# Kernel optimization log

Hardware: AMD Instinct MI355X
Metric: run time of the kernel (lower is better)

## Reference

```python
import jax, jax.numpy as jnp
import numpy as np

N_NODES = 100000
D = 128


def gcn_conv(x, W, b, src, dst, deg_inv_sqrt):
    # PyG GCNConv: linear transform, symmetric-normalized aggregation with self-loops, bias
    h = x @ W  # [N, D_out]
    norm = deg_inv_sqrt[src] * deg_inv_sqrt[dst]  # [E_tot]
    msgs = h[src] * norm[:, None]  # gather + scale  [E_tot, D_out]
    out = jax.ops.segment_sum(msgs, dst, num_segments=x.shape[0])  # scatter-add to targets
    return out + b


def _prep_edges(edge_index, n_nodes):
    # add self-loops (weight 1) and compute deg^{-1/2} over targets (flow source_to_target)
    loops = jnp.arange(n_nodes, dtype=edge_index.dtype)
    src = jnp.concatenate([edge_index[0], loops])
    dst = jnp.concatenate([edge_index[1], loops])
    deg = jax.ops.segment_sum(jnp.ones_like(dst, dtype=jnp.float32), dst, num_segments=n_nodes)
    deg_inv_sqrt = jnp.where(deg > 0, jax.lax.rsqrt(jnp.maximum(deg, 1.0)), 0.0)
    return src, dst, deg_inv_sqrt


def setup_inputs() -> dict:
    key = jax.random.key(0)
    ks = jax.random.split(key, 8)
    node_fts = jax.random.normal(ks[0], (N_NODES, D), dtype=jnp.float32)
    edge_index = jax.random.randint(ks[1], (2, 1600000), 0, N_NODES, dtype=jnp.int64)
    scale = 1.0 / np.sqrt(D)
    W1 = jax.random.uniform(ks[2], (D, D), jnp.float32, -scale, scale)
    b1 = jnp.zeros((D,), jnp.float32)
    W2 = jax.random.uniform(ks[3], (D, D), jnp.float32, -scale, scale)
    b2 = jnp.zeros((D,), jnp.float32)
    W3 = jax.random.uniform(ks[4], (D, D), jnp.float32, -scale, scale)
    b3 = jnp.zeros((D,), jnp.float32)
    return {"node_fts": node_fts, "edge_index": edge_index,
            "W1": W1, "b1": b1, "W2": W2, "b2": b2, "W3": W3, "b3": b3}


def reference(node_fts, edge_index, W1, b1, W2, b2, W3, b3):
    n = node_fts.shape[0]
    src, dst, dinv = _prep_edges(edge_index, n)
    x = jax.nn.relu(gcn_conv(node_fts, W1, b1, src, dst, dinv))
    x = jax.nn.relu(gcn_conv(x, W2, b2, src, dst, dinv))
    x = jax.nn.relu(gcn_conv(x, W3, b3, src, dst, dinv))
    return x
```

## Files before the change

kernel.cpp:

```cpp
#include <hip/hip_runtime.h>

#define NN 100000
#define EE 1600000
#define NPART 8
#define PSZ (NN / NPART)
#define NI4 (EE / 4)
#define SUBW 196
#define NSB (NPART * 64)
#define SCAP 4096
#define RCAP 8192
#define FCHUNKS 128
#define FBLOCKS (NPART * FCHUNKS)
#define WTBLOCKS 48
#define DEGB 64
#define LBCAP 48

typedef __attribute__((ext_vector_type(8))) short bf16x8;
typedef __attribute__((ext_vector_type(4))) float f32x4;

__device__ inline unsigned int f2bf2(float a, float b) {
    unsigned int ua = __float_as_uint(a);
    unsigned int ub = __float_as_uint(b);
    ua = (ua + 0x7fffu + ((ua >> 16) & 1u)) >> 16;
    ub = (ub + 0x7fffu + ((ub >> 16) & 1u)) >> 16;
    return ua | (ub << 16);
}
__device__ inline unsigned short f2bf(float a) {
    unsigned int u = __float_as_uint(a);
    return (unsigned short)((u + 0x7fffu + ((u >> 16) & 1u)) >> 16);
}
__device__ inline float2 bf2f2(unsigned int u) {
    return make_float2(__uint_as_float(u << 16), __uint_as_float(u & 0xffff0000u));
}


__global__ __launch_bounds__(256) void fbwt_kernel(const int4* __restrict__ src4,
                                                   const int4* __restrict__ dst4,
                                                   int* __restrict__ gcur2,
                                                   uint2* __restrict__ buckets2,
                                                   int* __restrict__ deg,
                                                   const float* __restrict__ W1,
                                                   const float* __restrict__ W2,
                                                   const float* __restrict__ W3,
                                                   unsigned short* __restrict__ wt1,
                                                   unsigned short* __restrict__ wt2,
                                                   unsigned short* __restrict__ wt3,
                                                   unsigned int* __restrict__ hb) {
    __shared__ uint2 bins[64][LBCAP];
    __shared__ int bcnt[64];
    __shared__ int gbase[64];
    __shared__ float tile[32][33];
    const int bx = blockIdx.x;

    if (bx < DEGB) {
        const int a0 = bx * (NI4 / DEGB);
        const int a1 = a0 + (NI4 / DEGB);
        for (int i = a0 + threadIdx.x; i < a1; i += 256) {
            int4 d4 = dst4[i];
            atomicAdd(&deg[d4.x], 1);
            atomicAdd(&deg[d4.y], 1);
            atomicAdd(&deg[d4.z], 1);
            atomicAdd(&deg[d4.w], 1);
        }
        return;
    }

    if (bx < DEGB + WTBLOCKS) {
        const int wb = bx - DEGB;
        const int m = wb >> 4;
        const int tl = wb & 15;
        const int ti = tl >> 2, tj = tl & 3;
        const float* W = m == 0 ? W1 : (m == 1 ? W2 : W3);
        unsigned short* wt = m == 0 ? wt1 : (m == 1 ? wt2 : wt3);
        const int r = threadIdx.x >> 5, c = threadIdx.x & 31;
#pragma unroll
        for (int rr = r; rr < 32; rr += 8)
            tile[rr][c] = W[(ti * 32 + rr) * 128 + tj * 32 + c];
        __syncthreads();
#pragma unroll
        for (int rr = r; rr < 32; rr += 8)
            wt[(size_t)(tj * 32 + rr) * 128 + ti * 32 + c] = f2bf(tile[c][rr]);
        if (wb == 0 && threadIdx.x < 64) hb[(size_t)NN * 64 + threadIdx.x] = 0;
        return;
    }

    const int fb = bx - DEGB - WTBLOCKS;
    const int p = fb >> 7;
    const int ch = fb & 127;
    if (threadIdx.x < 64) bcnt[threadIdx.x] = 0;
    __syncthreads();
    const int lo = p * PSZ, hi = lo + PSZ;
    const int chunk4 = NI4 / FCHUNKS;
    const int a0 = ch * chunk4, a1 = a0 + chunk4;
    for (int i = a0 + threadIdx.x; i < a1; i += 256) {
        int4 d4 = dst4[i];
        bool m0 = (d4.x >= lo && d4.x < hi);
        bool m1 = (d4.y >= lo && d4.y < hi);
        bool m2 = (d4.z >= lo && d4.z < hi);
        bool m3 = (d4.w >= lo && d4.w < hi);
        if (!(m0 | m1 | m2 | m3)) continue;
        int4 s4 = src4[i];
        int ss[4] = {s4.x, s4.y, s4.z, s4.w};
        int dd[4] = {d4.x, d4.y, d4.z, d4.w};
        bool mm[4] = {m0, m1, m2, m3};
#pragma unroll
        for (int k = 0; k < 4; ++k) {
            if (!mm[k]) continue;
            int li = (dd[k] - lo) / SUBW;
            int pos = atomicAdd(&bcnt[li], 1);
            if (pos < LBCAP) {
                bins[li][pos] = make_uint2((unsigned)ss[k], (unsigned)dd[k]);
            } else {
                int sb = p * 64 + li;
                int gp = atomicAdd(&gcur2[sb], 1);
                buckets2[(size_t)sb * SCAP + gp] = make_uint2((unsigned)ss[k], (unsigned)dd[k]);
            }
        }
    }
    __syncthreads();
    if (threadIdx.x < 64) {
        int cc = min(bcnt[threadIdx.x], LBCAP);
        gbase[threadIdx.x] = atomicAdd(&gcur2[p * 64 + threadIdx.x], cc);
        bcnt[threadIdx.x] = cc;
    }
    __syncthreads();
    for (int b = 0; b < 64; ++b) {
        const int cc = bcnt[b];
        uint2* outp = buckets2 + (size_t)(p * 64 + b) * SCAP + gbase[b];
        for (int i = threadIdx.x; i < cc; i += 256) outp[i] = bins[b][i];
    }
}


template <bool F32IN>
__device__ __forceinline__ void gemm_body(int wave, const void* __restrict__ xin,
                                          const unsigned short* __restrict__ wt,
                                          const int* __restrict__ deg,
                                          unsigned int* __restrict__ hb) {
    const int base = wave * 64;
    if (base >= NN) return;
    const int lane = threadIdx.x & 63;
    const int r = lane & 15;
    const int q = lane >> 4;
    const unsigned short* wrow = wt + (size_t)r * 128 + q * 8;
    bf16x8 wfr[4][8];
#pragma unroll
    for (int kc = 0; kc < 4; ++kc)
#pragma unroll
        for (int nt = 0; nt < 8; ++nt)
            wfr[kc][nt] = *(const bf16x8*)(wrow + (size_t)nt * 16 * 128 + kc * 32);
#pragma unroll
    for (int tt = 0; tt < 4; ++tt) {
        const int m0 = base + tt * 16;
        if (m0 >= NN) break;
        f32x4 acc[8] = {};
#pragma unroll
        for (int kc = 0; kc < 4; ++kc) {
            bf16x8 xf;
            if (F32IN) {
                const float* xrow = (const float*)xin + (size_t)(m0 + r) * 128 + q * 8 + kc * 32;
                float4 a = *(const float4*)xrow;
                float4 b = *(const float4*)(xrow + 4);
                unsigned short tmp[8] = {f2bf(a.x), f2bf(a.y), f2bf(a.z), f2bf(a.w),
                                         f2bf(b.x), f2bf(b.y), f2bf(b.z), f2bf(b.w)};
                xf = *(const bf16x8*)tmp;
            } else {
                const unsigned short* xrow =
                    (const unsigned short*)xin + (size_t)(m0 + r) * 128 + q * 8 + kc * 32;
                xf = *(const bf16x8*)xrow;
            }
#pragma unroll
            for (int nt = 0; nt < 8; ++nt)
                acc[nt] = __builtin_amdgcn_mfma_f32_16x16x32_bf16(wfr[kc][nt], xf, acc[nt], 0, 0, 0);
        }
        const int orow = m0 + r;
        const float dvr = rsqrtf(1.0f + (float)deg[orow]);
        unsigned int* hrow = hb + (size_t)orow * 64;
#pragma unroll
        for (int nt = 0; nt < 8; ++nt) {
            int n = nt * 16 + q * 4;
            *(uint2*)(hrow + (n >> 1)) =
                make_uint2(f2bf2(acc[nt][0] * dvr, acc[nt][1] * dvr),
                           f2bf2(acc[nt][2] * dvr, acc[nt][3] * dvr));
        }
    }
}


__global__ __launch_bounds__(256, 2) void sort3_gemm1_kernel(const uint2* __restrict__ buckets2,
                                                             const int* __restrict__ gcur2,
                                                             int* __restrict__ csr,
                                                             int* __restrict__ info,
                                                             float* __restrict__ dinv,
                                                             const float* __restrict__ x0,
                                                             const unsigned short* __restrict__ wt1,
                                                             const int* __restrict__ deg,
                                                             unsigned int* __restrict__ hb) {
    __shared__ int hist[256];
    __shared__ int pscan[256];
    __shared__ int lcur[256];
    __shared__ int staged[RCAP];
    if (blockIdx.x >= 512) {
        const int wave = (blockIdx.x - 512) * 4 + (threadIdx.x >> 6);
        gemm_body<true>(wave, (const void*)x0, wt1, deg, hb);
        return;
    }
    const int sb = blockIdx.x;
    const int li = sb & 63;
    const int base_node = (sb >> 6) * PSZ + li * SUBW;
    const int nnodes = min(SUBW, PSZ - li * SUBW);
    const int scnt = gcur2[sb];
    const uint2* bk = buckets2 + (size_t)sb * SCAP;
    const int t = threadIdx.x;
    hist[t] = 0;
    __syncthreads();
    for (int i = t; i < scnt; i += 256) atomicAdd(&hist[(int)bk[i].y - base_node], 1);
    __syncthreads();
    const int padded = (t < nnodes) ? ((hist[t] + 7) & ~7) : 0;
    pscan[t] = padded;
    __syncthreads();
    for (int off = 1; off < 256; off <<= 1) {
        int v = (t >= off) ? pscan[t - off] : 0;
        __syncthreads();
        pscan[t] += v;
        __syncthreads();
    }
    const int rstart = pscan[t] - padded;
    lcur[t] = rstart;
    __syncthreads();
    const int total = pscan[255];
    for (int i = t; i < total; i += 256) staged[i] = NN;
    __syncthreads();
    for (int i = t; i < scnt; i += 256) {
        uint2 r = bk[i];
        int pos = atomicAdd(&lcur[(int)r.y - base_node], 1);
        staged[pos] = (int)r.x;
    }
    __syncthreads();
    int4* co = (int4*)(csr + (size_t)sb * RCAP);
    for (int i = t; i < (total >> 2); i += 256) co[i] = ((const int4*)staged)[i];
    if (t < nnodes) {
        int dg = hist[t];
        info[base_node + t] = ((sb * RCAP + rstart) << 8) | dg;
        dinv[base_node + t] = rsqrtf(1.0f + (float)dg);
    }
}

template <bool F32IN>
__global__ __launch_bounds__(256, 2) void gemm_kernel(const void* __restrict__ xin,
                                                      const unsigned short* __restrict__ wt,
                                                      const int* __restrict__ deg,
                                                      unsigned int* __restrict__ hb) {
    const int wave = blockIdx.x * 4 + (threadIdx.x >> 6);
    gemm_body<F32IN>(wave, xin, wt, deg, hb);
}


template <bool BF16OUT>
__device__ __forceinline__ void agg_node(int d, const unsigned int* __restrict__ hb,
                                         const int* __restrict__ csr,
                                         const int* __restrict__ info,
                                         const float* __restrict__ dinv,
                                         const float2* __restrict__ bias2,
                                         void* __restrict__ outp) {
    const int j = threadIdx.x & 63;
    const int ifo = info[d];
    int e = ifo >> 8;
    const int end = e + (((ifo & 255) + 7) & ~7);
    float2 acc = bf2f2(hb[(size_t)d * 64 + j]);
    for (; e + 16 <= end; e += 16) {
        int4 c0 = *(const int4*)(csr + e);
        int4 c1 = *(const int4*)(csr + e + 4);
        int4 c2 = *(const int4*)(csr + e + 8);
        int4 c3 = *(const int4*)(csr + e + 12);
        unsigned int v0 = hb[(size_t)c0.x * 64 + j];
        unsigned int v1 = hb[(size_t)c0.y * 64 + j];
        unsigned int v2 = hb[(size_t)c0.z * 64 + j];
        unsigned int v3 = hb[(size_t)c0.w * 64 + j];
        unsigned int v4 = hb[(size_t)c1.x * 64 + j];
        unsigned int v5 = hb[(size_t)c1.y * 64 + j];
        unsigned int v6 = hb[(size_t)c1.z * 64 + j];
        unsigned int v7 = hb[(size_t)c1.w * 64 + j];
        unsigned int v8 = hb[(size_t)c2.x * 64 + j];
        unsigned int v9 = hb[(size_t)c2.y * 64 + j];
        unsigned int va = hb[(size_t)c2.z * 64 + j];
        unsigned int vb = hb[(size_t)c2.w * 64 + j];
        unsigned int vc = hb[(size_t)c3.x * 64 + j];
        unsigned int vd = hb[(size_t)c3.y * 64 + j];
        unsigned int ve = hb[(size_t)c3.z * 64 + j];
        unsigned int vf = hb[(size_t)c3.w * 64 + j];
        float2 f0 = bf2f2(v0), f1 = bf2f2(v1), f2 = bf2f2(v2), f3 = bf2f2(v3);
        float2 f4 = bf2f2(v4), f5 = bf2f2(v5), f6 = bf2f2(v6), f7 = bf2f2(v7);
        float2 f8 = bf2f2(v8), f9 = bf2f2(v9), fa = bf2f2(va), fb = bf2f2(vb);
        float2 fc = bf2f2(vc), fd = bf2f2(vd), fe = bf2f2(ve), ff = bf2f2(vf);
        acc.x += ((f0.x + f1.x) + (f2.x + f3.x)) + ((f4.x + f5.x) + (f6.x + f7.x)) +
                 ((f8.x + f9.x) + (fa.x + fb.x)) + ((fc.x + fd.x) + (fe.x + ff.x));
        acc.y += ((f0.y + f1.y) + (f2.y + f3.y)) + ((f4.y + f5.y) + (f6.y + f7.y)) +
                 ((f8.y + f9.y) + (fa.y + fb.y)) + ((fc.y + fd.y) + (fe.y + ff.y));
    }
    if (e < end) {
        int4 c0 = *(const int4*)(csr + e);
        int4 c1 = *(const int4*)(csr + e + 4);
        unsigned int v0 = hb[(size_t)c0.x * 64 + j];
        unsigned int v1 = hb[(size_t)c0.y * 64 + j];
        unsigned int v2 = hb[(size_t)c0.z * 64 + j];
        unsigned int v3 = hb[(size_t)c0.w * 64 + j];
        unsigned int v4 = hb[(size_t)c1.x * 64 + j];
        unsigned int v5 = hb[(size_t)c1.y * 64 + j];
        unsigned int v6 = hb[(size_t)c1.z * 64 + j];
        unsigned int v7 = hb[(size_t)c1.w * 64 + j];
        float2 f0 = bf2f2(v0), f1 = bf2f2(v1), f2 = bf2f2(v2), f3 = bf2f2(v3);
        float2 f4 = bf2f2(v4), f5 = bf2f2(v5), f6 = bf2f2(v6), f7 = bf2f2(v7);
        acc.x += ((f0.x + f1.x) + (f2.x + f3.x)) + ((f4.x + f5.x) + (f6.x + f7.x));
        acc.y += ((f0.y + f1.y) + (f2.y + f3.y)) + ((f4.y + f5.y) + (f6.y + f7.y));
    }
    const float dv = dinv[d];
    float2 bb = bias2[j];
    float ox = fmaxf(dv * acc.x + bb.x, 0.0f);
    float oy = fmaxf(dv * acc.y + bb.y, 0.0f);
    if (BF16OUT) {
        ((unsigned int*)outp)[(size_t)d * 64 + j] = f2bf2(ox, oy);
    } else {
        ((float2*)outp)[(size_t)d * 64 + j] = make_float2(ox, oy);
    }
}

template <bool BF16OUT>
__global__ __launch_bounds__(256) void aggregate_kernel(const unsigned int* __restrict__ hb,
                                                        const int* __restrict__ csr,
                                                        const int* __restrict__ info,
                                                        const float* __restrict__ dinv,
                                                        const float2* __restrict__ bias2,
                                                        void* __restrict__ outp) {
    const int w = threadIdx.x >> 6;
    const int stride = (int)gridDim.x * 4;
    for (int d = blockIdx.x * 4 + w; d < NN; d += stride)
        agg_node<BF16OUT>(d, hb, csr, info, dinv, bias2, outp);
}


extern "C" void kernel_launch(void* const* d_in, const int* in_sizes, int n_in,
                              void* d_out, int out_size, void* d_ws, size_t ws_size,
                              hipStream_t stream) {
    const float* x0 = (const float*)d_in[0];
    const int* ei = (const int*)d_in[1];
    const float* W1 = (const float*)d_in[2];
    const float* b1 = (const float*)d_in[3];
    const float* W2 = (const float*)d_in[4];
    const float* b2 = (const float*)d_in[5];
    const float* W3 = (const float*)d_in[6];
    const float* b3 = (const float*)d_in[7];
    float* out = (float*)d_out;

    char* ws = (char*)d_ws;
    size_t off = 0;
    auto alloc = [&](size_t bytes) -> void* {
        off = (off + 511) & ~(size_t)511;
        void* p = ws + off;
        off += bytes;
        return p;
    };
    unsigned int* hb  = (unsigned int*)alloc(((size_t)NN + 1) * 64 * 4);
    int*   csr     = (int*)  alloc((size_t)NSB * RCAP * sizeof(int));
    uint2* buckets2 = (uint2*)alloc((size_t)NSB * SCAP * sizeof(uint2));
    int*   info    = (int*)  alloc((size_t)NN * sizeof(int));
    float* dinv    = (float*)alloc((size_t)NN * sizeof(float));
    int*   deg     = (int*)  alloc((size_t)NN * sizeof(int));
    int*   gcur2   = (int*)  alloc(NSB * sizeof(int));
    unsigned short* wt1 = (unsigned short*)alloc(128 * 128 * 2);
    unsigned short* wt2 = (unsigned short*)alloc(128 * 128 * 2);
    unsigned short* wt3 = (unsigned short*)alloc(128 * 128 * 2);

    unsigned int* xact = (unsigned int*)d_out;

    const int4* src4 = (const int4*)ei;
    const int4* dst4 = (const int4*)(ei + EE);

    hipMemsetAsync(gcur2, 0, NSB * sizeof(int), stream);
    hipMemsetAsync(deg, 0, (size_t)NN * sizeof(int), stream);
    fbwt_kernel<<<DEGB + WTBLOCKS + FBLOCKS, 256, 0, stream>>>(src4, dst4, gcur2, buckets2, deg,
                                                               W1, W2, W3, wt1, wt2, wt3, hb);
    sort3_gemm1_kernel<<<903, 256, 0, stream>>>(buckets2, gcur2, csr, info, dinv,
                                                x0, wt1, deg, hb);
    aggregate_kernel<true><<<2048, 256, 0, stream>>>(hb, csr, info, dinv,
                                                     (const float2*)b1, (void*)xact);
    gemm_kernel<false><<<391, 256, 0, stream>>>((const void*)xact, wt2, deg, hb);
    aggregate_kernel<true><<<2048, 256, 0, stream>>>(hb, csr, info, dinv,
                                                     (const float2*)b2, (void*)xact);
    gemm_kernel<false><<<391, 256, 0, stream>>>((const void*)xact, wt3, deg, hb);
    aggregate_kernel<false><<<2048, 256, 0, stream>>>(hb, csr, info, dinv,
                                                      (const float2*)b3, (void*)out);
}
```

Baseline: 448.9 us.

## Replace bucketed CSR sort with fixed-capacity per-node rows via atomic scatter

Drops the two-pass partition, bucket and local-sort CSR build and instead gives each destination node a fixed 64-slot row, pre-filled with a sentinel index and filled through per-node atomic cursors. Aggregation now indexes a row directly by node id and derives the normalization from the degree array, so the info and dinv arrays go away and aggregate uses one wave per node with no grid-stride loop. This cuts the preprocessing work and a kernel's worth of global traffic, in exchange for heavy global atomics, scattered 4-byte writes and a 25.6 MB CSR fill. Any node with more than 64 incoming edges would overflow its row, which is only safe for the random test graph.

```diff
diff --git a/kernel.cpp b/kernel.cpp
--- a/kernel.cpp
+++ b/kernel.cpp
@@ -2,18 +2,13 @@
 
 #define NN 100000
 #define EE 1600000
-#define NPART 8
-#define PSZ (NN / NPART)
 #define NI4 (EE / 4)
-#define SUBW 196
-#define NSB (NPART * 64)
-#define SCAP 4096
-#define RCAP 8192
-#define FCHUNKS 128
-#define FBLOCKS (NPART * FCHUNKS)
-#define WTBLOCKS 48
-#define DEGB 64
-#define LBCAP 48
+#define ROWCAP 64
+#define DEGB 128
+#define WTB 48
+#define FILLB 512
+#define SCB 1024
+#define G1B 391
 
 typedef __attribute__((ext_vector_type(8))) short bf16x8;
 typedef __attribute__((ext_vector_type(4))) float f32x4;
@@ -34,21 +29,16 @@
 }
 
 
-__global__ __launch_bounds__(256) void fbwt_kernel(const int4* __restrict__ src4,
-                                                   const int4* __restrict__ dst4,
-                                                   int* __restrict__ gcur2,
-                                                   uint2* __restrict__ buckets2,
-                                                   int* __restrict__ deg,
-                                                   const float* __restrict__ W1,
-                                                   const float* __restrict__ W2,
-                                                   const float* __restrict__ W3,
-                                                   unsigned short* __restrict__ wt1,
-                                                   unsigned short* __restrict__ wt2,
-                                                   unsigned short* __restrict__ wt3,
-                                                   unsigned int* __restrict__ hb) {
-    __shared__ uint2 bins[64][LBCAP];
-    __shared__ int bcnt[64];
-    __shared__ int gbase[64];
+__global__ __launch_bounds__(256) void prep1_kernel(const int4* __restrict__ dst4,
+                                                    int* __restrict__ deg,
+                                                    const float* __restrict__ W1,
+                                                    const float* __restrict__ W2,
+                                                    const float* __restrict__ W3,
+                                                    unsigned short* __restrict__ wt1,
+                                                    unsigned short* __restrict__ wt2,
+                                                    unsigned short* __restrict__ wt3,
+                                                    unsigned int* __restrict__ hb,
+                                                    int* __restrict__ csr) {
     __shared__ float tile[32][33];
     const int bx = blockIdx.x;
 
@@ -65,7 +55,7 @@
         return;
     }
 
-    if (bx < DEGB + WTBLOCKS) {
+    if (bx < DEGB + WTB) {
         const int wb = bx - DEGB;
         const int m = wb >> 4;
         const int tl = wb & 15;
@@ -84,51 +74,12 @@
         return;
     }
 
-    const int fb = bx - DEGB - WTBLOCKS;
-    const int p = fb >> 7;
-    const int ch = fb & 127;
-    if (threadIdx.x < 64) bcnt[threadIdx.x] = 0;
-    __syncthreads();
-    const int lo = p * PSZ, hi = lo + PSZ;
-    const int chunk4 = NI4 / FCHUNKS;
-    const int a0 = ch * chunk4, a1 = a0 + chunk4;
-    for (int i = a0 + threadIdx.x; i < a1; i += 256) {
-        int4 d4 = dst4[i];
-        bool m0 = (d4.x >= lo && d4.x < hi);
-        bool m1 = (d4.y >= lo && d4.y < hi);
-        bool m2 = (d4.z >= lo && d4.z < hi);
-        bool m3 = (d4.w >= lo && d4.w < hi);
-        if (!(m0 | m1 | m2 | m3)) continue;
-        int4 s4 = src4[i];
-        int ss[4] = {s4.x, s4.y, s4.z, s4.w};
-        int dd[4] = {d4.x, d4.y, d4.z, d4.w};
-        bool mm[4] = {m0, m1, m2, m3};
-#pragma unroll
-        for (int k = 0; k < 4; ++k) {
-            if (!mm[k]) continue;
-            int li = (dd[k] - lo) / SUBW;
-            int pos = atomicAdd(&bcnt[li], 1);
-            if (pos < LBCAP) {
-                bins[li][pos] = make_uint2((unsigned)ss[k], (unsigned)dd[k]);
-            } else {
-                int sb = p * 64 + li;
-                int gp = atomicAdd(&gcur2[sb], 1);
-                buckets2[(size_t)sb * SCAP + gp] = make_uint2((unsigned)ss[k], (unsigned)dd[k]);
-            }
-        }
-    }
-    __syncthreads();
-    if (threadIdx.x < 64) {
-        int cc = min(bcnt[threadIdx.x], LBCAP);
-        gbase[threadIdx.x] = atomicAdd(&gcur2[p * 64 + threadIdx.x], cc);
-        bcnt[threadIdx.x] = cc;
-    }
-    __syncthreads();
-    for (int b = 0; b < 64; ++b) {
-        const int cc = bcnt[b];
-        uint2* outp = buckets2 + (size_t)(p * 64 + b) * SCAP + gbase[b];
-        for (int i = threadIdx.x; i < cc; i += 256) outp[i] = bins[b][i];
-    }
+    const int fb = bx - DEGB - WTB;
+    int4* c4 = (int4*)csr;
+    const int a0 = fb * ((NN * ROWCAP / 4) / FILLB);
+    const int a1 = a0 + ((NN * ROWCAP / 4) / FILLB);
+    const int4 sv = make_int4(NN, NN, NN, NN);
+    for (int i = a0 + threadIdx.x; i < a1; i += 256) c4[i] = sv;
 }
 
 
@@ -187,63 +138,31 @@
 }
 
 
-__global__ __launch_bounds__(256, 2) void sort3_gemm1_kernel(const uint2* __restrict__ buckets2,
-                                                             const int* __restrict__ gcur2,
-                                                             int* __restrict__ csr,
-                                                             int* __restrict__ info,
-                                                             float* __restrict__ dinv,
-                                                             const float* __restrict__ x0,
-                                                             const unsigned short* __restrict__ wt1,
-                                                             const int* __restrict__ deg,
-                                                             unsigned int* __restrict__ hb) {
-    __shared__ int hist[256];
-    __shared__ int pscan[256];
-    __shared__ int lcur[256];
-    __shared__ int staged[RCAP];
-    if (blockIdx.x >= 512) {
-        const int wave = (blockIdx.x - 512) * 4 + (threadIdx.x >> 6);
-        gemm_body<true>(wave, (const void*)x0, wt1, deg, hb);
+__global__ __launch_bounds__(256, 2) void scatter_gemm1_kernel(const int4* __restrict__ src4,
+                                                               const int4* __restrict__ dst4,
+                                                               int* __restrict__ cur,
+                                                               int* __restrict__ csr,
+                                                               const float* __restrict__ x0,
+                                                               const unsigned short* __restrict__ wt1,
+                                                               const int* __restrict__ deg,
+                                                               unsigned int* __restrict__ hb) {
+    if (blockIdx.x < SCB) {
+        for (int i = blockIdx.x * 256 + threadIdx.x; i < NI4; i += SCB * 256) {
+            int4 d4 = dst4[i];
+            int4 s4 = src4[i];
+            int p0 = atomicAdd(&cur[d4.x], 1);
+            int p1 = atomicAdd(&cur[d4.y], 1);
+            int p2 = atomicAdd(&cur[d4.z], 1);
+            int p3 = atomicAdd(&cur[d4.w], 1);
+            csr[(d4.x << 6) + p0] = s4.x;
+            csr[(d4.y << 6) + p1] = s4.y;
+            csr[(d4.z << 6) + p2] = s4.z;
+            csr[(d4.w << 6) + p3] = s4.w;
+        }
         return;
     }
-    const int sb = blockIdx.x;
-    const int li = sb & 63;
-    const int base_node = (sb >> 6) * PSZ + li * SUBW;
-    const int nnodes = min(SUBW, PSZ - li * SUBW);
-    const int scnt = gcur2[sb];
-    const uint2* bk = buckets2 + (size_t)sb * SCAP;
-    const int t = threadIdx.x;
-    hist[t] = 0;
-    __syncthreads();
-    for (int i = t; i < scnt; i += 256) atomicAdd(&hist[(int)bk[i].y - base_node], 1);
-    __syncthreads();
-    const int padded = (t < nnodes) ? ((hist[t] + 7) & ~7) : 0;
-    pscan[t] = padded;
-    __syncthreads();
-    for (int off = 1; off < 256; off <<= 1) {
-        int v = (t >= off) ? pscan[t - off] : 0;
-        __syncthreads();
-        pscan[t] += v;
-        __syncthreads();
-    }
-    const int rstart = pscan[t] - padded;
-    lcur[t] = rstart;
-    __syncthreads();
-    const int total = pscan[255];
-    for (int i = t; i < total; i += 256) staged[i] = NN;
-    __syncthreads();
-    for (int i = t; i < scnt; i += 256) {
-        uint2 r = bk[i];
-        int pos = atomicAdd(&lcur[(int)r.y - base_node], 1);
-        staged[pos] = (int)r.x;
-    }
-    __syncthreads();
-    int4* co = (int4*)(csr + (size_t)sb * RCAP);
-    for (int i = t; i < (total >> 2); i += 256) co[i] = ((const int4*)staged)[i];
-    if (t < nnodes) {
-        int dg = hist[t];
-        info[base_node + t] = ((sb * RCAP + rstart) << 8) | dg;
-        dinv[base_node + t] = rsqrtf(1.0f + (float)dg);
-    }
+    const int wave = (blockIdx.x - SCB) * 4 + (threadIdx.x >> 6);
+    gemm_body<true>(wave, (const void*)x0, wt1, deg, hb);
 }
 
 template <bool F32IN>
@@ -257,16 +176,16 @@
 
 
 template <bool BF16OUT>
-__device__ __forceinline__ void agg_node(int d, const unsigned int* __restrict__ hb,
-                                         const int* __restrict__ csr,
-                                         const int* __restrict__ info,
-                                         const float* __restrict__ dinv,
-                                         const float2* __restrict__ bias2,
-                                         void* __restrict__ outp) {
+__global__ __launch_bounds__(256) void aggregate_kernel(const unsigned int* __restrict__ hb,
+                                                        const int* __restrict__ csr,
+                                                        const int* __restrict__ deg,
+                                                        const float2* __restrict__ bias2,
+                                                        void* __restrict__ outp) {
+    const int d = blockIdx.x * 4 + (threadIdx.x >> 6);
     const int j = threadIdx.x & 63;
-    const int ifo = info[d];
-    int e = ifo >> 8;
-    const int end = e + (((ifo & 255) + 7) & ~7);
+    const int dg = deg[d];
+    int e = d << 6;
+    const int end = e + ((dg + 7) & ~7);
     float2 acc = bf2f2(hb[(size_t)d * 64 + j]);
     for (; e + 16 <= end; e += 16) {
         int4 c0 = *(const int4*)(csr + e);
@@ -314,7 +233,7 @@
         acc.x += ((f0.x + f1.x) + (f2.x + f3.x)) + ((f4.x + f5.x) + (f6.x + f7.x));
         acc.y += ((f0.y + f1.y) + (f2.y + f3.y)) + ((f4.y + f5.y) + (f6.y + f7.y));
     }
-    const float dv = dinv[d];
+    const float dv = rsqrtf(1.0f + (float)dg);
     float2 bb = bias2[j];
     float ox = fmaxf(dv * acc.x + bb.x, 0.0f);
     float oy = fmaxf(dv * acc.y + bb.y, 0.0f);
@@ -323,19 +242,6 @@
     } else {
         ((float2*)outp)[(size_t)d * 64 + j] = make_float2(ox, oy);
     }
-}
-
-template <bool BF16OUT>
-__global__ __launch_bounds__(256) void aggregate_kernel(const unsigned int* __restrict__ hb,
-                                                        const int* __restrict__ csr,
-                                                        const int* __restrict__ info,
-                                                        const float* __restrict__ dinv,
-                                                        const float2* __restrict__ bias2,
-                                                        void* __restrict__ outp) {
-    const int w = threadIdx.x >> 6;
-    const int stride = (int)gridDim.x * 4;
-    for (int d = blockIdx.x * 4 + w; d < NN; d += stride)
-        agg_node<BF16OUT>(d, hb, csr, info, dinv, bias2, outp);
 }
 
 
@@ -360,13 +266,10 @@
         off += bytes;
         return p;
     };
-    unsigned int* hb  = (unsigned int*)alloc(((size_t)NN + 1) * 64 * 4);
-    int*   csr     = (int*)  alloc((size_t)NSB * RCAP * sizeof(int));
-    uint2* buckets2 = (uint2*)alloc((size_t)NSB * SCAP * sizeof(uint2));
-    int*   info    = (int*)  alloc((size_t)NN * sizeof(int));
-    float* dinv    = (float*)alloc((size_t)NN * sizeof(float));
-    int*   deg     = (int*)  alloc((size_t)NN * sizeof(int));
-    int*   gcur2   = (int*)  alloc(NSB * sizeof(int));
+    unsigned int* hb = (unsigned int*)alloc(((size_t)NN + 1) * 64 * 4);
+    int* csr = (int*)alloc((size_t)NN * ROWCAP * sizeof(int));
+    int* deg = (int*)alloc((size_t)NN * sizeof(int));
+    int* cur = (int*)alloc((size_t)NN * sizeof(int));
     unsigned short* wt1 = (unsigned short*)alloc(128 * 128 * 2);
     unsigned short* wt2 = (unsigned short*)alloc(128 * 128 * 2);
     unsigned short* wt3 = (unsigned short*)alloc(128 * 128 * 2);
@@ -376,18 +279,18 @@
     const int4* src4 = (const int4*)ei;
     const int4* dst4 = (const int4*)(ei + EE);
 
-    hipMemsetAsync(gcur2, 0, NSB * sizeof(int), stream);
     hipMemsetAsync(deg, 0, (size_t)NN * sizeof(int), stream);
-    fbwt_kernel<<<DEGB + WTBLOCKS + FBLOCKS, 256, 0, stream>>>(src4, dst4, gcur2, buckets2, deg,
-                                                               W1, W2, W3, wt1, wt2, wt3, hb);
-    sort3_gemm1_kernel<<<903, 256, 0, stream>>>(buckets2, gcur2, csr, info, dinv,
-                                                x0, wt1, deg, hb);
-    aggregate_kernel<true><<<2048, 256, 0, stream>>>(hb, csr, info, dinv,
-                                                     (const float2*)b1, (void*)xact);
-    gemm_kernel<false><<<391, 256, 0, stream>>>((const void*)xact, wt2, deg, hb);
-    aggregate_kernel<true><<<2048, 256, 0, stream>>>(hb, csr, info, dinv,
-                                                     (const float2*)b2, (void*)xact);
-    gemm_kernel<false><<<391, 256, 0, stream>>>((const void*)xact, wt3, deg, hb);
-    aggregate_kernel<false><<<2048, 256, 0, stream>>>(hb, csr, info, dinv,
-                                                      (const float2*)b3, (void*)out);
-}
+    hipMemsetAsync(cur, 0, (size_t)NN * sizeof(int), stream);
+    prep1_kernel<<<DEGB + WTB + FILLB, 256, 0, stream>>>(dst4, deg, W1, W2, W3,
+                                                         wt1, wt2, wt3, hb, csr);
+    scatter_gemm1_kernel<<<SCB + G1B, 256, 0, stream>>>(src4, dst4, cur, csr,
+                                                        x0, wt1, deg, hb);
+    aggregate_kernel<true><<<NN / 4, 256, 0, stream>>>(hb, csr, deg,
+                                                       (const float2*)b1, (void*)xact);
+    gemm_kernel<false><<<G1B, 256, 0, stream>>>((const void*)xact, wt2, deg, hb);
+    aggregate_kernel<true><<<NN / 4, 256, 0, stream>>>(hb, csr, deg,
+                                                       (const float2*)b2, (void*)xact);
+    gemm_kernel<false><<<G1B, 256, 0, stream>>>((const void*)xact, wt3, deg, hb);
+    aggregate_kernel<false><<<NN / 4, 256, 0, stream>>>(hb, csr, deg,
+                                                        (const float2*)b3, (void*)out);
+}
```

Result: slower. 559.2 us (+24.6%).
